# Kernel tuning notes

Measured on AMD Instinct MI355X. Metric: run time of the kernel, lower is better.

## Reference

```python
import jax, jax.numpy as jnp
import numpy as np

DISCOUNT_FACTOR = 0.99
ADVANTAGE_LAMBDA = 0.95
LAMBD_GRAD_SCALE = 0.5


def setup_inputs() -> dict:
    key = jax.random.key(0)
    k1, k2, k3 = jax.random.split(key, 3)
    B, T, D = 4096, 2048, 1
    values = jax.random.normal(k1, (B, T + 1, D), dtype=jnp.float32)
    rewards = jax.random.normal(k2, (B, T, D), dtype=jnp.float32)
    # binary terminal flags (float, as in the torch module: used as (1 - dones))
    dones = (jax.random.uniform(k3, (B, T, D)) < 0.02).astype(jnp.float32)
    raw_gamma = jnp.zeros((1,), dtype=jnp.float32)
    raw_lambd = jnp.zeros((T,), dtype=jnp.float32)
    return {
        "values": values,
        "rewards": rewards,
        "dones": dones,
        "raw_gamma": raw_gamma,
        "raw_lambd": raw_lambd,
        "start_idx": 0,
        "end_idx": T,
    }


def reference(values, rewards, dones, raw_gamma, raw_lambd, start_idx, end_idx):
    # dynamic gamma / lambda (sigmoid-reparameterized around the base values)
    gamma = DISCOUNT_FACTOR + (1.0 - DISCOUNT_FACTOR) * (2.0 * jax.nn.sigmoid(raw_gamma) - 1.0)
    dyn_lambd = ADVANTAGE_LAMBDA + (1.0 - ADVANTAGE_LAMBDA) * (2.0 * jax.nn.sigmoid(raw_lambd) - 1.0)
    # GradScaler(scale=0.5): forward identity, gradient scaled by 0.5
    lambd = LAMBD_GRAD_SCALE * dyn_lambd + jax.lax.stop_gradient((1.0 - LAMBD_GRAD_SCALE) * dyn_lambd)
    g = gamma[0]
    td_l = lambd[start_idx:end_idx]                      # [T]

    # time-major views for the reverse-time scan
    r_tm = jnp.moveaxis(rewards, 1, 0)                   # [T, B, D]
    d_tm = jnp.moveaxis(dones, 1, 0)                     # [T, B, D]
    vn_tm = jnp.moveaxis(values[:, 1:, :], 1, 0)         # [T, B, D] = values[t+1]

    def step(carry, x):
        sum_r, lam_ret = carry
        r, d, vn, l = x
        cont = g * (1.0 - d)
        # torch computes sum_rewards under no_grad -> stop_gradient here
        new_sum = jax.lax.stop_gradient(r + cont * (l * sum_r))
        new_lam = r + cont * ((1.0 - l) * vn + l * lam_ret)
        return (new_sum, new_lam), (new_sum, new_lam)

    init = (jnp.zeros_like(values[:, -1, :]), values[:, -1, :])
    _, (sums_tm, lams_tm) = jax.lax.scan(step, init, (r_tm, d_tm, vn_tm, td_l), reverse=True)

    lambda_returns = jnp.concatenate(
        [jnp.moveaxis(lams_tm, 0, 1), values[:, -1:, :]], axis=1
    )                                                    # [B, T+1, D]
    sum_rewards = jnp.moveaxis(sums_tm, 0, 1)            # [B, T, D] (== torch sum_rewards[:, :-1])
    return lambda_returns, sum_rewards
```

## Files before the change

kernel.cpp:

```cpp
#include <hip/hip_runtime.h>


struct Aff { float aL, aS, b; };

__device__ inline Aff compose(const Aff& L, const Aff& R) {
    Aff o;
    o.aL = fmaf(L.b, R.aL, L.aL);
    o.aS = fmaf(L.b, R.aS, L.aS);
    o.b  = L.b * R.b;
    return o;
}

__global__ void lam_precompute(const float* __restrict__ raw_lambd,
                               const int* __restrict__ start_p,
                               float* __restrict__ lam, int T) {
    int t = blockIdx.x * blockDim.x + threadIdx.x;
    if (t < T) lam[t] = 0.9f + 0.1f / (1.0f + __expf(-raw_lambd[start_p[0] + t]));
}

__global__ __launch_bounds__(512)
void td_scan_kernel(const float* __restrict__ values,
                    const float* __restrict__ rewards,
                    const float* __restrict__ dones,
                    const float* __restrict__ raw_gamma,
                    const float* __restrict__ lam_arr,
                    float* __restrict__ out,
                    int B, int T)
{
    const int b    = blockIdx.x;
    const int tid  = threadIdx.x;
    const int lane = tid & 63;
    const int wave = tid >> 6;
    const int nwaves = blockDim.x >> 6;

    __shared__ float s_wAL[8], s_wAS[8], s_wB[8];
    __shared__ float s_cL[8], s_cS[8];
    __shared__ float s_vT;

    const float g = 0.98f + 0.02f / (1.0f + __expf(-raw_gamma[0]));

    const float* vrow = values  + (size_t)b * (T + 1);
    const float* rrow = rewards + (size_t)b * T;
    const float* drow = dones   + (size_t)b * T;
    float* lam_out = out + (size_t)b * (T + 1);
    float* sum_out = out + (size_t)B * (T + 1) + (size_t)b * T;

    const int base = tid * 4;

    float r[4], d[4], l[4], vn[4];
    const bool full = (base + 3) < T;
    if (full) {
        const float4 r4 = *(const float4*)(rrow + base);
        const float4 d4 = *(const float4*)(drow + base);
        const float4 l4 = *(const float4*)(lam_arr + base);
        r[0]=r4.x; r[1]=r4.y; r[2]=r4.z; r[3]=r4.w;
        d[0]=d4.x; d[1]=d4.y; d[2]=d4.z; d[3]=d4.w;
        l[0]=l4.x; l[1]=l4.y; l[2]=l4.z; l[3]=l4.w;
        vn[0]=vrow[base+1]; vn[1]=vrow[base+2]; vn[2]=vrow[base+3]; vn[3]=vrow[base+4];
    } else {
        #pragma unroll
        for (int k = 0; k < 4; ++k) {
            const int t = base + k;
            r[k] = (t < T) ? rrow[t] : 0.0f;
            d[k] = (t < T) ? drow[t] : 1.0f;
            l[k] = (t < T) ? lam_arr[t] : 0.0f;
            vn[k] = (t < T) ? vrow[t + 1] : 0.0f;
        }
    }
    if (tid == 0) {
        float vT = vrow[T];
        s_vT = vT;
        lam_out[T] = vT;
    }

    Aff M[4];
    #pragma unroll
    for (int k = 0; k < 4; ++k) {
        const int t = base + k;
        if (t < T) {
            const float cont = g * (1.0f - d[k]);
            M[k].b  = cont * l[k];
            M[k].aL = fmaf(cont * (1.0f - l[k]), vn[k], r[k]);
            M[k].aS = r[k];
        } else {
            M[k].aL = 0.0f; M[k].aS = 0.0f; M[k].b = 1.0f;
        }
    }
    Aff C = M[3];
    C = compose(M[2], C);
    C = compose(M[1], C);
    C = compose(M[0], C);

    Aff S = C;
    #pragma unroll
    for (int dlt = 1; dlt < 64; dlt <<= 1) {
        Aff oth;
        oth.aL = __shfl_down(S.aL, dlt, 64);
        oth.aS = __shfl_down(S.aS, dlt, 64);
        oth.b  = __shfl_down(S.b,  dlt, 64);
        if (lane + dlt < 64) S = compose(S, oth);
    }
    Aff E;
    E.aL = __shfl_down(S.aL, 1, 64);
    E.aS = __shfl_down(S.aS, 1, 64);
    E.b  = __shfl_down(S.b,  1, 64);
    if (lane == 63) { E.aL = 0.0f; E.aS = 0.0f; E.b = 1.0f; }

    if (lane == 0) { s_wAL[wave] = S.aL; s_wAS[wave] = S.aS; s_wB[wave] = S.b; }
    __syncthreads();

    if (tid == 0) {
        float cL = s_vT, cS = 0.0f;
        for (int w = nwaves - 1; w >= 0; --w) {
            s_cL[w] = cL; s_cS[w] = cS;
            const float wb = s_wB[w];
            cL = fmaf(wb, cL, s_wAL[w]);
            cS = fmaf(wb, cS, s_wAS[w]);
        }
    }
    __syncthreads();

    const float cwL = s_cL[wave];
    const float cwS = s_cS[wave];
    float xL = fmaf(E.b, cwL, E.aL);
    float xS = fmaf(E.b, cwS, E.aS);

    float oL[4], oS[4];
    #pragma unroll
    for (int k = 3; k >= 0; --k) {
        xL = fmaf(M[k].b, xL, M[k].aL);
        xS = fmaf(M[k].b, xS, M[k].aS);
        oL[k] = xL; oS[k] = xS;
    }

    if (full) {
        *(float4*)(sum_out + base) = make_float4(oS[0], oS[1], oS[2], oS[3]);
        lam_out[base + 0] = oL[0];
        lam_out[base + 1] = oL[1];
        lam_out[base + 2] = oL[2];
        lam_out[base + 3] = oL[3];
    } else {
        #pragma unroll
        for (int k = 0; k < 4; ++k) {
            const int t = base + k;
            if (t < T) { lam_out[t] = oL[k]; sum_out[t] = oS[k]; }
        }
    }
}

extern "C" void kernel_launch(void* const* d_in, const int* in_sizes, int n_in,
                              void* d_out, int out_size, void* d_ws, size_t ws_size,
                              hipStream_t stream) {
    const float* values    = (const float*)d_in[0];
    const float* rewards   = (const float*)d_in[1];
    const float* dones     = (const float*)d_in[2];
    const float* raw_gamma = (const float*)d_in[3];
    const float* raw_lambd = (const float*)d_in[4];
    const int*   start_idx = (const int*)d_in[5];
    float* out = (float*)d_out;
    float* lam_arr = (float*)d_ws;

    const int n_values  = in_sizes[0];
    const int n_rewards = in_sizes[1];
    const int B = n_values - n_rewards;
    const int T = n_rewards / B;

    lam_precompute<<<(T + 255) / 256, 256, 0, stream>>>(raw_lambd, start_idx, lam_arr, T);
    td_scan_kernel<<<B, 512, 0, stream>>>(values, rewards, dones, raw_gamma,
                                          lam_arr, out, B, T);
}
```

Measured before the change: 153.9 us.

## Stage misaligned value rows through LDS for vectorized loads and stores

```diff
diff --git a/kernel.cpp b/kernel.cpp
--- a/kernel.cpp
+++ b/kernel.cpp
@@ -1,5 +1,10 @@
 #include <hip/hip_runtime.h>
 
+
+#define TPB 256
+#define EPT 8
+
+typedef float v4f __attribute__((ext_vector_type(4)));
 
 struct Aff { float aL, aS, b; };
 
@@ -11,85 +16,94 @@
     return o;
 }
 
-__global__ void lam_precompute(const float* __restrict__ raw_lambd,
-                               const int* __restrict__ start_p,
-                               float* __restrict__ lam, int T) {
+__global__ void precompute_kernel(const float* __restrict__ raw_gamma,
+                                  const float* __restrict__ raw_lambd,
+                                  const int* __restrict__ start_p,
+                                  float* __restrict__ lam, int T) {
     int t = blockIdx.x * blockDim.x + threadIdx.x;
     if (t < T) lam[t] = 0.9f + 0.1f / (1.0f + __expf(-raw_lambd[start_p[0] + t]));
-}
-
-__global__ __launch_bounds__(512)
+    if (t == 0) lam[T] = 0.98f + 0.02f / (1.0f + __expf(-raw_gamma[0]));
+}
+
+__global__ __launch_bounds__(TPB, 8)
 void td_scan_kernel(const float* __restrict__ values,
                     const float* __restrict__ rewards,
                     const float* __restrict__ dones,
-                    const float* __restrict__ raw_gamma,
                     const float* __restrict__ lam_arr,
                     float* __restrict__ out,
                     int B, int T)
 {
+    __shared__ __align__(16) float s_buf[2064];
+    __shared__ float s_wAL[4], s_wAS[4], s_wB[4], s_cL[4], s_cS[4];
+
     const int b    = blockIdx.x;
     const int tid  = threadIdx.x;
     const int lane = tid & 63;
     const int wave = tid >> 6;
-    const int nwaves = blockDim.x >> 6;
-
-    __shared__ float s_wAL[8], s_wAS[8], s_wB[8];
-    __shared__ float s_cL[8], s_cS[8];
-    __shared__ float s_vT;
-
-    const float g = 0.98f + 0.02f / (1.0f + __expf(-raw_gamma[0]));
-
-    const float* vrow = values  + (size_t)b * (T + 1);
+    const int nwaves = TPB >> 6;
+
+    const float g = lam_arr[T];
+
+    const size_t rowV = (size_t)b * (T + 1);
     const float* rrow = rewards + (size_t)b * T;
     const float* drow = dones   + (size_t)b * T;
-    float* lam_out = out + (size_t)b * (T + 1);
-    float* sum_out = out + (size_t)B * (T + 1) + (size_t)b * T;
-
-    const int base = tid * 4;
-
-    float r[4], d[4], l[4], vn[4];
-    const bool full = (base + 3) < T;
-    if (full) {
-        const float4 r4 = *(const float4*)(rrow + base);
-        const float4 d4 = *(const float4*)(drow + base);
-        const float4 l4 = *(const float4*)(lam_arr + base);
-        r[0]=r4.x; r[1]=r4.y; r[2]=r4.z; r[3]=r4.w;
-        d[0]=d4.x; d[1]=d4.y; d[2]=d4.z; d[3]=d4.w;
-        l[0]=l4.x; l[1]=l4.y; l[2]=l4.z; l[3]=l4.w;
-        vn[0]=vrow[base+1]; vn[1]=vrow[base+2]; vn[2]=vrow[base+3]; vn[3]=vrow[base+4];
-    } else {
-        #pragma unroll
-        for (int k = 0; k < 4; ++k) {
-            const int t = base + k;
-            r[k] = (t < T) ? rrow[t] : 0.0f;
-            d[k] = (t < T) ? drow[t] : 1.0f;
-            l[k] = (t < T) ? lam_arr[t] : 0.0f;
-            vn[k] = (t < T) ? vrow[t + 1] : 0.0f;
-        }
-    }
-    if (tid == 0) {
-        float vT = vrow[T];
-        s_vT = vT;
-        lam_out[T] = vT;
-    }
-
-    Aff M[4];
-    #pragma unroll
-    for (int k = 0; k < 4; ++k) {
-        const int t = base + k;
-        if (t < T) {
-            const float cont = g * (1.0f - d[k]);
-            M[k].b  = cont * l[k];
-            M[k].aL = fmaf(cont * (1.0f - l[k]), vn[k], r[k]);
-            M[k].aS = r[k];
+
+    const size_t firstNeeded = rowV + 1;
+    const int off = (int)(firstNeeded & 3);
+    const size_t A = firstNeeded - off;
+    const int nStage = T + off;
+    const int n4 = (nStage + 3) >> 2;
+    const size_t totalElems = (size_t)B * (T + 1);
+    for (int j = tid; j < n4; j += TPB) {
+        const size_t gb = A + 4 * (size_t)j;
+        if (gb + 3 < totalElems) {
+            *(v4f*)(s_buf + 4 * j) = *(const v4f*)(values + gb);
         } else {
-            M[k].aL = 0.0f; M[k].aS = 0.0f; M[k].b = 1.0f;
-        }
-    }
-    Aff C = M[3];
-    C = compose(M[2], C);
-    C = compose(M[1], C);
-    C = compose(M[0], C);
+            #pragma unroll
+            for (int c = 0; c < 4; ++c)
+                s_buf[4 * j + c] = (gb + c < totalElems) ? values[gb + c] : 0.0f;
+        }
+    }
+    __syncthreads();
+
+    const float vT = s_buf[off + T - 1];
+
+    const int base = tid * EPT;
+    float r[EPT], d[EPT], l[EPT], vn[EPT];
+    {
+        const v4f r0 = *(const v4f*)(rrow + base);
+        const v4f r1 = *(const v4f*)(rrow + base + 4);
+        const v4f d0 = *(const v4f*)(drow + base);
+        const v4f d1 = *(const v4f*)(drow + base + 4);
+        const v4f l0 = *(const v4f*)(lam_arr + base);
+        const v4f l1 = *(const v4f*)(lam_arr + base + 4);
+        r[0]=r0.x; r[1]=r0.y; r[2]=r0.z; r[3]=r0.w; r[4]=r1.x; r[5]=r1.y; r[6]=r1.z; r[7]=r1.w;
+        d[0]=d0.x; d[1]=d0.y; d[2]=d0.z; d[3]=d0.w; d[4]=d1.x; d[5]=d1.y; d[6]=d1.z; d[7]=d1.w;
+        l[0]=l0.x; l[1]=l0.y; l[2]=l0.z; l[3]=l0.w; l[4]=l1.x; l[5]=l1.y; l[6]=l1.z; l[7]=l1.w;
+    }
+    {
+        const v4f w0 = *(const v4f*)(s_buf + base);
+        const v4f w1 = *(const v4f*)(s_buf + base + 4);
+        const v4f w2 = *(const v4f*)(s_buf + base + 8);
+        switch (off) {
+        case 0: vn[0]=w0.x; vn[1]=w0.y; vn[2]=w0.z; vn[3]=w0.w; vn[4]=w1.x; vn[5]=w1.y; vn[6]=w1.z; vn[7]=w1.w; break;
+        case 1: vn[0]=w0.y; vn[1]=w0.z; vn[2]=w0.w; vn[3]=w1.x; vn[4]=w1.y; vn[5]=w1.z; vn[6]=w1.w; vn[7]=w2.x; break;
+        case 2: vn[0]=w0.z; vn[1]=w0.w; vn[2]=w1.x; vn[3]=w1.y; vn[4]=w1.z; vn[5]=w1.w; vn[6]=w2.x; vn[7]=w2.y; break;
+        default: vn[0]=w0.w; vn[1]=w1.x; vn[2]=w1.y; vn[3]=w1.z; vn[4]=w1.w; vn[5]=w2.x; vn[6]=w2.y; vn[7]=w2.z; break;
+        }
+    }
+
+    Aff M[EPT];
+    #pragma unroll
+    for (int k = 0; k < EPT; ++k) {
+        const float cont = g * (1.0f - d[k]);
+        M[k].b  = cont * l[k];
+        M[k].aL = fmaf(cont * (1.0f - l[k]), vn[k], r[k]);
+        M[k].aS = r[k];
+    }
+    Aff C = M[EPT - 1];
+    #pragma unroll
+    for (int k = EPT - 2; k >= 0; --k) C = compose(M[k], C);
 
     Aff S = C;
     #pragma unroll
@@ -110,7 +124,7 @@
     __syncthreads();
 
     if (tid == 0) {
-        float cL = s_vT, cS = 0.0f;
+        float cL = vT, cS = 0.0f;
         for (int w = nwaves - 1; w >= 0; --w) {
             s_cL[w] = cL; s_cS[w] = cS;
             const float wb = s_wB[w];
@@ -124,28 +138,47 @@
     const float cwS = s_cS[wave];
     float xL = fmaf(E.b, cwL, E.aL);
     float xS = fmaf(E.b, cwS, E.aS);
-
-    float oL[4], oS[4];
-    #pragma unroll
-    for (int k = 3; k >= 0; --k) {
+    float oL[EPT], oS[EPT];
+    #pragma unroll
+    for (int k = EPT - 1; k >= 0; --k) {
         xL = fmaf(M[k].b, xL, M[k].aL);
         xS = fmaf(M[k].b, xS, M[k].aS);
         oL[k] = xL; oS[k] = xS;
     }
 
-    if (full) {
-        *(float4*)(sum_out + base) = make_float4(oS[0], oS[1], oS[2], oS[3]);
-        lam_out[base + 0] = oL[0];
-        lam_out[base + 1] = oL[1];
-        lam_out[base + 2] = oL[2];
-        lam_out[base + 3] = oL[3];
-    } else {
-        #pragma unroll
-        for (int k = 0; k < 4; ++k) {
-            const int t = base + k;
-            if (t < T) { lam_out[t] = oL[k]; sum_out[t] = oS[k]; }
-        }
-    }
+    float* sum_out = out + (size_t)B * (T + 1) + (size_t)b * T;
+    {
+        v4f s0 = { oS[0], oS[1], oS[2], oS[3] };
+        v4f s1 = { oS[4], oS[5], oS[6], oS[7] };
+        __builtin_nontemporal_store(s0, (v4f*)(sum_out + base));
+        __builtin_nontemporal_store(s1, (v4f*)(sum_out + base + 4));
+    }
+
+    #pragma unroll
+    for (int k = 0; k < EPT; ++k) s_buf[base + k] = oL[k];
+    if (tid == 0) s_buf[T] = vT;
+    __syncthreads();
+
+    const size_t O = (size_t)b * (T + 1);
+    const int sh = (int)((4 - (O & 3)) & 3);
+    if (tid < sh) out[O + tid] = s_buf[tid];
+    const int rem  = T + 1 - sh;
+    const int m4   = rem >> 2;
+    const int tail = rem & 3;
+    for (int j = tid; j < m4; j += TPB) {
+        const int ls = sh + 4 * j;
+        const v4f lo = *(const v4f*)(s_buf + (ls - sh));
+        const v4f hi = *(const v4f*)(s_buf + (ls - sh) + 4);
+        v4f v;
+        switch (sh) {
+        case 0:  v = lo; break;
+        case 1:  v = (v4f){ lo.y, lo.z, lo.w, hi.x }; break;
+        case 2:  v = (v4f){ lo.z, lo.w, hi.x, hi.y }; break;
+        default: v = (v4f){ lo.w, hi.x, hi.y, hi.z }; break;
+        }
+        __builtin_nontemporal_store(v, (v4f*)(out + O + ls));
+    }
+    if (tid < tail) { const int ls = sh + 4 * m4 + tid; out[O + ls] = s_buf[ls]; }
 }
 
 extern "C" void kernel_launch(void* const* d_in, const int* in_sizes, int n_in,
@@ -165,7 +198,7 @@
     const int B = n_values - n_rewards;
     const int T = n_rewards / B;
 
-    lam_precompute<<<(T + 255) / 256, 256, 0, stream>>>(raw_lambd, start_idx, lam_arr, T);
-    td_scan_kernel<<<B, 512, 0, stream>>>(values, rewards, dones, raw_gamma,
-                                          lam_arr, out, B, T);
-}
+    precompute_kernel<<<(T + 256) / 256, 256, 0, stream>>>(raw_gamma, raw_lambd,
+                                                           start_idx, lam_arr, T);
+    td_scan_kernel<<<B, TPB, 0, stream>>>(values, rewards, dones, lam_arr, out, B, T);
+}
```

Measured after the change: 158.6 us. 3.1% more time.
